# Kernel tuning notes

Measured on AMD Instinct MI355X. Metric: run time of the kernel, lower is better.

Reference implementation:

```python
import jax, jax.numpy as jnp
import numpy as np

N = 50000      # nodes
E = 800000     # edges (avg degree 16)
IN = 128       # in_feats
OUT = 128      # out_feats
ASSIGN = 256   # assign_dim = B graphs * 8 clusters
B = 32         # batch_size (num graphs)


def setup_inputs() -> dict:
    key = jax.random.key(0)
    k0, k1, k2, k3 = jax.random.split(key, 4)
    x = jax.random.normal(k0, (N, IN), jnp.float32)
    edge_index = jax.random.randint(k1, (2, E), 0, N, dtype=jnp.int32)
    # sorted graph ids, ~equal-sized graphs (mirrors block_diag mask construction)
    batch = ((jnp.arange(N, dtype=jnp.int32) * B) // N).astype(jnp.int32)
    # SAGEConv params: Linear(2*in_feats -> out) on concat([x, mean_neigh])
    W_embed = jax.random.normal(k2, (2 * IN, OUT), jnp.float32) / np.float32(np.sqrt(2 * IN))
    b_embed = jnp.zeros((OUT,), jnp.float32)
    W_pool = jax.random.normal(k3, (2 * IN, ASSIGN), jnp.float32) / np.float32(np.sqrt(2 * IN))
    b_pool = jnp.zeros((ASSIGN,), jnp.float32)
    return dict(x=x, edge_index=edge_index, batch=batch,
                W_embed=W_embed, b_embed=b_embed, W_pool=W_pool, b_pool=b_pool)


def _sage(x, src, dst, W, b):
    # mean aggregation over in-neighbors (messages src -> dst), then Linear on concat
    n = x.shape[0]
    deg = jax.ops.segment_sum(jnp.ones((src.shape[0],), x.dtype), dst, num_segments=n)
    neigh = jax.ops.segment_sum(x[src], dst, num_segments=n) / jnp.maximum(deg, 1.0)[:, None]
    return jnp.concatenate([x, neigh], axis=-1) @ W + b


def reference(x, edge_index, batch, W_embed, b_embed, W_pool, b_pool):
    src, dst = edge_index[0], edge_index[1]
    embed = _sage(x, src, dst, W_embed, b_embed)                      # [N, OUT]
    pooled = jax.nn.softmax(_sage(x, src, dst, W_pool, b_pool), -1)   # [N, ASSIGN]
    # block-diagonal mask: node i of graph g sees columns [g*C, (g+1)*C)
    C = ASSIGN // B
    cols = jnp.arange(ASSIGN, dtype=batch.dtype) // C
    mask = (batch[:, None] == cols[None, :]).astype(x.dtype)          # [N, ASSIGN]
    # NOTE: faithful to original: softmax of (mask * pooled), zeros contribute exp(0)
    r = jax.nn.softmax(mask * pooled, axis=-1) * mask
    r = r / (r.sum(axis=-1, keepdims=True) + 1e-13)                   # [N, ASSIGN]
    h = r.T @ embed                                                   # [ASSIGN, OUT]
    # adj_new = S^T A S with A sparse COO (rows=edge_index[0], cols=edge_index[1])
    ar = jax.ops.segment_sum(r[dst], src, num_segments=x.shape[0])    # A @ S : [N, ASSIGN]
    adj_new = r.T @ ar                                                # [ASSIGN, ASSIGN]
    return (adj_new, h)
```

## Files before the change

### kernel.cpp

```cpp
#include <hip/hip_runtime.h>
#include <hip/hip_bf16.h>

#define N_ 50000
#define E_ 800000
#define IN_ 128
#define OUT_ 128
#define ASSIGN_ 256
#define B_ 32
#define KTOT 256
#define JTOT 384
#define HCHUNK 32
#define ACHUNK 32
#define AST 72
#define NXP ((N_ + 127) / 128)
#define NGB (NXP * 3)
#define NCVX 6250

#define NBKT 256
#define NPB 196
#define BCAP 4000
#define EPB 4096
#define NBLK_A ((E_ + EPB - 1) / EPB)
#define NPRE (NBLK_A + NCVX + 384)

typedef __attribute__((ext_vector_type(8))) short short8;
typedef __attribute__((ext_vector_type(4))) float f32x4;
typedef __attribute__((ext_vector_type(2))) float f32x2;
typedef __attribute__((ext_vector_type(4))) unsigned short ushort4v;
typedef __attribute__((ext_vector_type(2))) unsigned short ushort2v;
typedef unsigned short u16;

__device__ inline unsigned short f2bf(float v) {
    union { float f; unsigned u; } a;
    a.f = v;
    unsigned r = a.u + 0x7fff + ((a.u >> 16) & 1);
    return (unsigned short)(r >> 16);
}
__device__ inline float bf2f(unsigned short b) {
    union { unsigned u; float f; } a;
    a.u = ((unsigned)b) << 16;
    return a.f;
}

__device__ inline unsigned enc8(float v) {
    union { float f; unsigned u; } a;
    a.f = v * 0x1p-120f;
    unsigned b = a.u;
    unsigned r = b + 0x7FFFF + ((b >> 20) & 1);
    return ((r >> 20) & 0x7F) | ((b >> 24) & 0x80);
}
__device__ inline float2 dec8x2(unsigned short p) {
#if defined(__has_builtin) && __has_builtin(__builtin_amdgcn_cvt_pk_f32_fp8)
    f32x2 r = __builtin_amdgcn_cvt_pk_f32_fp8((int)(unsigned)p, false);
    return make_float2(r.x, r.y);
#else
    unsigned u0 = p & 0xffu, u1 = (p >> 8) & 0xffu;
    union { unsigned u; float f; } a, b;
    a.u = ((u0 & 0x80u) << 24) | ((u0 & 0x7fu) << 20);
    b.u = ((u1 & 0x80u) << 24) | ((u1 & 0x7fu) << 20);
    return make_float2(a.f * 0x1p+120f, b.f * 0x1p+120f);
#endif
}

__device__ __forceinline__ void gload16(const u16* g, u16* l) {
    __builtin_amdgcn_global_load_lds(
        (const __attribute__((address_space(1))) void*)g,
        (__attribute__((address_space(3))) void*)l, 16, 0, 0);
}

__global__ __launch_bounds__(256) void k_pre(const int* __restrict__ ei,
                                             int* __restrict__ bktFill,
                                             int2* __restrict__ ebkt,
                                             const float* __restrict__ x,
                                             unsigned short* __restrict__ xhi,
                                             unsigned char* __restrict__ xq,
                                             const float* __restrict__ We,
                                             const float* __restrict__ be,
                                             const float* __restrict__ Wp,
                                             const float* __restrict__ bp,
                                             unsigned short* __restrict__ WThi,
                                             float* __restrict__ bias) {
    __shared__ int lh[NBKT], lbase[NBKT], lofs[NBKT];
    int bid = blockIdx.x;
    int t = threadIdx.x;
    if (bid < NBLK_A) {
        int e0 = bid * EPB;
        lh[t] = 0; lofs[t] = 0;
        __syncthreads();
        int ss[16], dd[16];
#pragma unroll
        for (int i = 0; i < 16; i++) {
            int e = e0 + i * 256 + t;
            ss[i] = 0; dd[i] = -1;
            if (e < E_) {
                ss[i] = ei[e];
                dd[i] = ei[E_ + e];
                atomicAdd(&lh[dd[i] / NPB], 1);
            }
        }
        __syncthreads();
        lbase[t] = t * BCAP + atomicAdd(&bktFill[t], lh[t]);
        __syncthreads();
#pragma unroll
        for (int i = 0; i < 16; i++) {
            if (dd[i] >= 0) {
                int b = dd[i] / NPB;
                int o = atomicAdd(&lofs[b], 1);
                ebkt[lbase[b] + o] = make_int2(ss[i], dd[i]);
            }
        }
        return;
    }
    if (bid >= NBLK_A + NCVX) {
        int idx = (bid - NBLK_A - NCVX) * 256 + t;
        if (idx < JTOT * KTOT) {
            int j = idx / KTOT, k = idx - j * KTOT;
            float v = (j < 128) ? We[k * 128 + j] : Wp[k * 256 + (j - 128)];
            WThi[idx] = f2bf(v);
        }
        if (idx < JTOT) bias[idx] = (idx < 128) ? be[idx] : bp[idx - 128];
        return;
    }
    int i4 = ((bid - NBLK_A) * 256 + t) * 4;
    if (i4 >= N_ * 128) return;
    float4 v = *(const float4*)(x + i4);
    ushort4v h;
    h.x = f2bf(v.x); h.y = f2bf(v.y); h.z = f2bf(v.z); h.w = f2bf(v.w);
    *(ushort4v*)(xhi + i4) = h;
    unsigned q = enc8(v.x) | (enc8(v.y) << 8) | (enc8(v.z) << 16) | (enc8(v.w) << 24);
    *(unsigned*)(xq + i4) = q;
}

__global__ __launch_bounds__(256) void k_binB(const int* __restrict__ bktFill,
                                              const int2* __restrict__ ebkt,
                                              int* __restrict__ ready,
                                              int* __restrict__ rowStart,
                                              int* __restrict__ csr_src,
                                              int* __restrict__ csr_dst) {
    __shared__ int ldeg[NPB];
    __shared__ int lscan[256];
    __shared__ int bsc[NBKT];
    __shared__ int lfill[NPB];
    int b = blockIdx.x, t = threadIdx.x;
    if (t < NPB) ldeg[t] = 0;
    __syncthreads();
    int base = b * BCAP;
    int cnt = bktFill[b];
    int n0 = b * NPB;
    for (int j = t; j < cnt; j += 256)
        atomicAdd(&ldeg[ebkt[base + j].y - n0], 1);
    __syncthreads();
    lscan[t] = (t < NPB) ? ldeg[t] : 0;
    __syncthreads();
    for (int off = 1; off < 256; off <<= 1) {
        int x0 = lscan[t];
        int a0 = (t >= off) ? lscan[t - off] : 0;
        __syncthreads();
        lscan[t] = x0 + a0;
        __syncthreads();
    }
    if (t == 0) atomicExch(&ready[b], lscan[NPB - 1] + 1);
    {
        int v;
        while ((v = atomicAdd(&ready[t], 0)) == 0) __builtin_amdgcn_s_sleep(8);
        bsc[t] = v - 1;
    }
    __syncthreads();
    for (int off = 1; off < NBKT; off <<= 1) {
        int x = bsc[t];
        int add = (t >= off) ? bsc[t - off] : 0;
        __syncthreads();
        bsc[t] = x + add;
        __syncthreads();
    }
    int base0 = (b == 0) ? 0 : bsc[b - 1];
    if (t < NPB) {
        int n = n0 + t;
        if (n < N_) {
            int excl = (t == 0) ? 0 : lscan[t - 1];
            lfill[t] = excl;
            rowStart[n] = base0 + excl;
        }
    }
    __syncthreads();
    for (int j = t; j < cnt; j += 256) {
        int2 sd = ebkt[base + j];
        int p = base0 + atomicAdd(&lfill[sd.y - n0], 1);
        csr_src[p] = sd.x;
        csr_dst[p] = sd.y;
    }
    if (b == 0 && t == 0) rowStart[N_] = E_;
}

__global__ __launch_bounds__(256) void k_agg(const unsigned char* __restrict__ xq,
                                             const int* __restrict__ rowStart,
                                             const int* __restrict__ csr_src,
                                             unsigned short* __restrict__ nhi) {
    int node = blockIdx.x * 4 + (threadIdx.x >> 6);
    if (node >= N_) return;
    int lane = threadIdx.x & 63;
    int es = lane >> 3;
    int fb = lane & 7;
    int a = rowStart[node], bnd = rowStart[node + 1];
    float acc[16];
#pragma unroll
    for (int k = 0; k < 16; k++) acc[k] = 0.f;
#define DEC(Q)                                                       \
    {                                                                \
        unsigned wq[4] = {(Q).x, (Q).y, (Q).z, (Q).w};               \
        _Pragma("unroll")                                            \
        for (int wi = 0; wi < 4; wi++) {                             \
            float2 f01 = dec8x2((unsigned short)(wq[wi] & 0xffffu)); \
            float2 f23 = dec8x2((unsigned short)(wq[wi] >> 16));     \
            acc[wi * 4 + 0] += f01.x; acc[wi * 4 + 1] += f01.y;      \
            acc[wi * 4 + 2] += f23.x; acc[wi * 4 + 3] += f23.y;      \
        }                                                            \
    }
    int j = a;
    for (; j + 8 < bnd; j += 16) {
        int s0 = csr_src[j + es];
        uint4 q0 = *(const uint4*)(xq + (size_t)s0 * 128 + fb * 16);
        uint4 q1 = {0, 0, 0, 0};
        int e1 = j + 8 + es;
        if (e1 < bnd) {
            int s1 = csr_src[e1];
            q1 = *(const uint4*)(xq + (size_t)s1 * 128 + fb * 16);
        }
        DEC(q0);
        DEC(q1);
    }
    if (j < bnd) {
        uint4 q0 = {0, 0, 0, 0};
        int e0 = j + es;
        if (e0 < bnd) {
            int s0 = csr_src[e0];
            q0 = *(const uint4*)(xq + (size_t)s0 * 128 + fb * 16);
        }
        DEC(q0);
    }
#undef DEC
#pragma unroll
    for (int k = 0; k < 16; k++) {
        acc[k] += __shfl_xor(acc[k], 8, 64);
        acc[k] += __shfl_xor(acc[k], 16, 64);
        acc[k] += __shfl_xor(acc[k], 32, 64);
    }
    float inv = 1.0f / (float)max(bnd - a, 1);
    if (es == 0) {
        short8 o0, o1;
#pragma unroll
        for (int k = 0; k < 8; k++) {
            o0[k] = (short)f2bf(acc[k] * inv);
            o1[k] = (short)f2bf(acc[k + 8] * inv);
        }
        *(short8*)(nhi + (size_t)node * 128 + fb * 16) = o0;
        *(short8*)(nhi + (size_t)node * 128 + fb * 16 + 8) = o1;
    }
}

__global__ __launch_bounds__(256) void k_gemm(const unsigned short* __restrict__ xhi,
                                              const unsigned short* __restrict__ nhi,
                                              const unsigned short* __restrict__ WThi,
                                              const float* __restrict__ bias,
                                              unsigned short* __restrict__ embed,
                                              unsigned short* __restrict__ plog) {
    __shared__ __align__(16) union {
        struct { u16 A[2][128 * 32]; u16 B[2][128 * 32]; } s;
        u16 ep[64 * 128];
    } sm;
    int t = threadIdx.x;
    int wave = t >> 6, lane = t & 63;
    int wm = wave >> 1, wn = wave & 1;
    int q = lane >> 4, lr = lane & 15;

    int id = blockIdx.x;
    int xi, cc;
    if (id < (NXP / 8) * 24) {
        xi = (id / 24) * 8 + (id & 7);
        cc = (id % 24) >> 3;
    } else {
        int r2 = id - (NXP / 8) * 24;
        xi = (NXP / 8) * 8 + r2 % (NXP % 8);
        cc = r2 / (NXP % 8);
    }
    int row0 = xi * 128;
    int col0 = cc * 128;

    f32x4 acc[4][4] = {};

    int segRow[2], segSl[2];
#pragma unroll
    for (int i = 0; i < 2; i++) {
        int R0 = (wave * 2 + i) * 16;
        segRow[i] = R0 + (lane >> 2);
        segSl[i] = (lane & 3) ^ ((segRow[i] >> 1) & 3);
    }

#define ISSUE(KT, BUF)                                                               \
    {                                                                                \
        const u16* Asrc = ((KT) < 128) ? xhi : nhi;                                  \
        int kb = (KT) & 127;                                                         \
        _Pragma("unroll")                                                            \
        for (int i = 0; i < 2; i++) {                                                \
            int nd = row0 + segRow[i];                                               \
            if (nd >= N_) nd = N_ - 1;                                               \
            gload16(Asrc + (size_t)nd * 128 + kb + segSl[i] * 8,                     \
                    &sm.s.A[BUF][((wave * 2 + i) * 16) * 32] + lane * 8);            \
            gload16(WThi + (size_t)(col0 + segRow[i]) * 256 + (KT) + segSl[i] * 8,   \
                    &sm.s.B[BUF][((wave * 2 + i) * 16) * 32] + lane * 8);            \
        }                                                                            \
    }

    ISSUE(0, 0);
    int p = 0;
    for (int kt = 0; kt < KTOT; kt += 32, p ^= 1) {
        __syncthreads();
        if (kt + 32 < KTOT) ISSUE(kt + 32, p ^ 1);

        short8 afh[4];
#pragma unroll
        for (int mi = 0; mi < 4; mi++) {
            int r = wm * 64 + mi * 16 + lr;
            afh[mi] = *(const short8*)&sm.s.A[p][r * 32 + ((q * 8) ^ (((r >> 1) & 3) * 8))];
        }
#pragma unroll
        for (int ni = 0; ni < 4; ni++) {
            int r = wn * 64 + ni * 16 + lr;
            short8 bfh = *(const short8*)&sm.s.B[p][r * 32 + ((q * 8) ^ (((r >> 1) & 3) * 8))];
#pragma unroll
            for (int mi = 0; mi < 4; mi++)
                acc[mi][ni] = __builtin_amdgcn_mfma_f32_16x16x32_bf16(afh[mi], bfh, acc[mi][ni], 0, 0, 0);
        }
    }
#undef ISSUE

    for (int half = 0; half < 2; half++) {
        __syncthreads();
        if (wm == half) {
#pragma unroll
            for (int mi = 0; mi < 4; mi++)
#pragma unroll
                for (int ni = 0; ni < 4; ni++) {
                    int lcol = wn * 64 + ni * 16 + lr;
                    float bj = bias[col0 + lcol];
#pragma unroll
                    for (int r = 0; r < 4; r++) {
                        int lrow = mi * 16 + q * 4 + r;
                        sm.ep[lrow * 128 + lcol] = f2bf(acc[mi][ni][r] + bj);
                    }
                }
        }
        __syncthreads();
#pragma unroll
        for (int i = 0; i < 4; i++) {
            int chunk = i * 256 + t;
            int lrow = chunk >> 4;
            int lco = (chunk & 15) * 8;
            int grow = row0 + half * 64 + lrow;
            if (grow < N_) {
                short8 v = *(const short8*)&sm.ep[lrow * 128 + lco];
                if (col0 < 128)
                    *(short8*)(embed + (size_t)grow * 128 + lco) = v;
                else
                    *(short8*)(plog + (size_t)grow * 256 + (col0 - 128) + lco) = v;
            }
        }
    }
}

__global__ __launch_bounds__(256) void k_r(const unsigned short* __restrict__ plog,
                                           const int* __restrict__ batch,
                                           float* __restrict__ r8,
                                           unsigned short* __restrict__ r8b) {
    int node = blockIdx.x * 4 + (threadIdx.x >> 6);
    int lane = threadIdx.x & 63;
    if (node >= N_) return;
    ushort4v p4 = *(const ushort4v*)(plog + (size_t)node * 256 + lane * 4);
    float px = bf2f(p4.x), py = bf2f(p4.y), pz = bf2f(p4.z), pw = bf2f(p4.w);
    float m = fmaxf(fmaxf(px, py), fmaxf(pz, pw));
    for (int off = 32; off; off >>= 1) m = fmaxf(m, __shfl_xor(m, off, 64));
    float s = expf(px - m) + expf(py - m) + expf(pz - m) + expf(pw - m);
    for (int off = 32; off; off >>= 1) s += __shfl_xor(s, off, 64);
    int g = batch[node];
    float v = 0.f;
    if (lane < 8) v = expf(bf2f(plog[(size_t)node * 256 + g * 8 + lane]) - m) / s;
    float M2 = v;
    for (int off = 4; off; off >>= 1) M2 = fmaxf(M2, __shfl_xor(M2, off, 64));
    float e = expf(v - M2);
    float Sg = e;
    for (int off = 4; off; off >>= 1) Sg += __shfl_xor(Sg, off, 64);
    float D2 = Sg + 248.0f * expf(-M2);
    float r = e / (Sg + 1e-13f * D2);
    if (lane < 8) {
        r8[node * 8 + lane] = r;
        r8b[node * 8 + lane] = f2bf(r);
    }
}

__global__ __launch_bounds__(256) void k_tail(const int* __restrict__ rowStart,
                                              const int* __restrict__ csr_src,
                                              const int* __restrict__ csr_dst,
                                              const unsigned short* __restrict__ r8b,
                                              float* __restrict__ partAdj,
                                              const unsigned short* __restrict__ embed,
                                              const float* __restrict__ r8,
                                              float* __restrict__ partH) {
    __shared__ __align__(16) unsigned short Ab[256 * AST];
    __shared__ __align__(16) unsigned short Bb[16 * AST];
    int id = blockIdx.x;
    int t = threadIdx.x;
    if (id >= B_ * ACHUNK) {
        int idh = id - B_ * ACHUNK;
        int g = idh & 31;
        int c = idh >> 5;
        int wv = t >> 6, l = t & 63;
        int n0g = (g * N_ + 31) >> 5;
        int n1g = ((g + 1) * N_ + 31) >> 5;
        int len = n1g - n0g;
        int a = n0g + (len * c) / HCHUNK;
        int b = n0g + (len * (c + 1)) / HCHUNK;
        float acc[8][2] = {};
        for (int n = a + wv; n < b; n += 4) {
            unsigned e2 = *(const unsigned*)(embed + (size_t)n * 128 + l * 2);
            float e0 = bf2f((u16)(e2 & 0xffffu));
            float e1 = bf2f((u16)(e2 >> 16));
            f32x4 r0 = *(const f32x4*)(r8 + n * 8);
            f32x4 r1 = *(const f32x4*)(r8 + n * 8 + 4);
#pragma unroll
            for (int c2 = 0; c2 < 4; c2++) {
                acc[c2][0] += r0[c2] * e0; acc[c2][1] += r0[c2] * e1;
                acc[c2 + 4][0] += r1[c2] * e0; acc[c2 + 4][1] += r1[c2] * e1;
            }
        }
        float* hredf = (float*)Ab;
#pragma unroll
        for (int c2 = 0; c2 < 8; c2++) {
            hredf[wv * 1024 + c2 * 128 + l * 2] = acc[c2][0];
            hredf[wv * 1024 + c2 * 128 + l * 2 + 1] = acc[c2][1];
        }
        __syncthreads();
        float* pb = partH + (g * HCHUNK + c) * 1024;
        for (int o = t; o < 1024; o += 256)
            pb[o] = (hredf[o] + hredf[1024 + o]) + (hredf[2048 + o] + hredf[3072 + o]);
        return;
    }
    int gd = id & 31;
    int c = id >> 5;
    int wave = t >> 6, lane = t & 63;
    int q = lane >> 4, lr = lane & 15;
    int n0g = (gd * N_ + 31) >> 5;
    int n1g = ((gd + 1) * N_ + 31) >> 5;
    int len = n1g - n0g;
    int na = n0g + (len * c) / ACHUNK;
    int nb = n0g + (len * (c + 1)) / ACHUNK;
    int j0 = rowStart[na], j1 = rowStart[nb];

    uint4 z = {0, 0, 0, 0};
#pragma unroll
    for (int i = 0; i < 9; i++) *(uint4*)&Ab[(i * 256 + t) * 8] = z;
    if (t < 144) *(uint4*)&Bb[t * 8] = z;
    __syncthreads();

    f32x4 acc[4] = {};
    int el = t >> 2;
    int ap = t & 3;

    int jcur = j0 + el;
    unsigned sv = 0, dv = 0;
    int gs = 0;
    bool have = jcur < j1;
    if (have) {
        int s = csr_src[jcur];
        int d = csr_dst[jcur];
        gs = (s * B_) / N_;
        sv = *(const unsigned*)(r8b + (size_t)s * 8 + ap * 2);
        dv = *(const unsigned*)(r8b + (size_t)d * 8 + ap * 2);
    }
    int pca = -1;

    for (int jt = j0; jt < j1; jt += 64) {
        if (pca >= 0) {
            Ab[pca * AST + el] = 0;
            Ab[(pca + 1) * AST + el] = 0;
            Bb[(ap * 2) * AST + el] = 0;
            Bb[(ap * 2 + 1) * AST + el] = 0;
        }
        int ca = -1;
        if (have) {
            ca = gs * 8 + ap * 2;
            Ab[ca * AST + el] = (unsigned short)sv;
            Ab[(ca + 1) * AST + el] = (unsigned short)(sv >> 16);
            Bb[(ap * 2) * AST + el] = (unsigned short)dv;
            Bb[(ap * 2 + 1) * AST + el] = (unsigned short)(dv >> 16);
        }
        __syncthreads();
        int jn = jt + 64 + el;
        bool haveN = jn < j1;
        unsigned svN = 0, dvN = 0;
        int gsN = 0;
        if (haveN) {
            int s = csr_src[jn];
            int d = csr_dst[jn];
            gsN = (s * B_) / N_;
            svN = *(const unsigned*)(r8b + (size_t)s * 8 + ap * 2);
            dvN = *(const unsigned*)(r8b + (size_t)d * 8 + ap * 2);
        }
        short8 bf0 = *(const short8*)&Bb[lr * AST + q * 8];
        short8 bf1 = *(const short8*)&Bb[lr * AST + 32 + q * 8];
#pragma unroll
        for (int mi = 0; mi < 4; mi++) {
            int col = (wave * 4 + mi) * 16 + lr;
            short8 a0 = *(const short8*)&Ab[col * AST + q * 8];
            short8 a1 = *(const short8*)&Ab[col * AST + 32 + q * 8];
            acc[mi] = __builtin_amdgcn_mfma_f32_16x16x32_bf16(a0, bf0, acc[mi], 0, 0, 0);
            acc[mi] = __builtin_amdgcn_mfma_f32_16x16x32_bf16(a1, bf1, acc[mi], 0, 0, 0);
        }
        __syncthreads();
        pca = ca;
        have = haveN; gs = gsN; sv = svN; dv = dvN;
    }

    float* pb = partAdj + (gd * ACHUNK + c) * 2048;
    if (lr < 8) {
#pragma unroll
        for (int mi = 0; mi < 4; mi++) {
            int mbase = (wave * 4 + mi) * 16 + q * 4;
#pragma unroll
            for (int r = 0; r < 4; r++)
                pb[(mbase + r) * 8 + lr] = acc[mi][r];
        }
    }
}

__global__ __launch_bounds__(256) void k_red(const float* __restrict__ partAdj,
                                             const float* __restrict__ partH,
                                             float* __restrict__ out) {
    int o = blockIdx.x * 256 + threadIdx.x;
    if (o < 256 * 256) {
        int row = o >> 8, col = o & 255;
        int gd = col >> 3, b = col & 7;
        int li = row * 8 + b;
        float s = 0.f;
#pragma unroll
        for (int c = 0; c < ACHUNK; c++) s += partAdj[(gd * ACHUNK + c) * 2048 + li];
        out[o] = s;
    } else {
        int idx = o - 256 * 256;
        int g = idx >> 10;
        int local = idx & 1023;
        float s = 0.f;
#pragma unroll
        for (int c = 0; c < HCHUNK; c++) s += partH[(g * HCHUNK + c) * 1024 + local];
        out[256 * 256 + idx] = s;
    }
}

extern "C" void kernel_launch(void* const* d_in, const int* in_sizes, int n_in,
                              void* d_out, int out_size, void* d_ws, size_t ws_size,
                              hipStream_t stream) {
    const float* x = (const float*)d_in[0];
    const int* ei = (const int*)d_in[1];
    const int* batch = (const int*)d_in[2];
    const float* We = (const float*)d_in[3];
    const float* be = (const float*)d_in[4];
    const float* Wp = (const float*)d_in[5];
    const float* bp = (const float*)d_in[6];
    float* out = (float*)d_out;

    char* w = (char*)d_ws;
    auto alloc = [&](size_t bytes) -> char* {
        char* p = w;
        w += (bytes + 255) & ~(size_t)255;
        return p;
    };
    unsigned short* xhi = (unsigned short*)alloc((size_t)N_ * 128 * 2);
    unsigned char* xq = (unsigned char*)alloc((size_t)N_ * 128);
    unsigned short* nhi = (unsigned short*)alloc((size_t)N_ * 128 * 2);
    unsigned short* WThi = (unsigned short*)alloc((size_t)JTOT * KTOT * 2);
    unsigned short* embed = (unsigned short*)alloc((size_t)N_ * 128 * 2);
    unsigned short* plog = (unsigned short*)alloc((size_t)N_ * 256 * 2);
    float* r8 = (float*)alloc((size_t)N_ * 8 * 4);
    unsigned short* r8b = (unsigned short*)alloc((size_t)N_ * 8 * 2);
    float* bias = (float*)alloc(JTOT * 4);
    int* rowStart = (int*)alloc((size_t)(N_ + 1) * 4);
    int* csr_src = (int*)alloc((size_t)E_ * 4);
    int* csr_dst = (int*)alloc((size_t)E_ * 4);
    int* flags = (int*)alloc(2 * NBKT * 4);
    int* bktFill = flags;
    int* ready = flags + NBKT;
    int2* ebkt = (int2*)alloc((size_t)NBKT * BCAP * 8);
    float* partH = (float*)alloc((size_t)B_ * HCHUNK * 1024 * 4);
    float* partAdj = (float*)alloc((size_t)B_ * ACHUNK * 2048 * 4);

    hipMemsetAsync(flags, 0, 2 * NBKT * 4, stream);
    k_pre<<<NPRE, 256, 0, stream>>>(ei, bktFill, ebkt, x, xhi, xq, We, be, Wp, bp, WThi, bias);
    k_binB<<<NBKT, 256, 0, stream>>>(bktFill, ebkt, ready, rowStart, csr_src, csr_dst);
    k_agg<<<(N_ + 3) / 4, 256, 0, stream>>>(xq, rowStart, csr_src, nhi);
    k_gemm<<<NGB, 256, 0, stream>>>(xhi, nhi, WThi, bias, embed, plog);
    k_r<<<(N_ + 3) / 4, 256, 0, stream>>>(plog, batch, r8, r8b);
    k_tail<<<2 * B_ * ACHUNK, 256, 0, stream>>>(rowStart, csr_src, csr_dst, r8b, partAdj,
                                                embed, r8, partH);
    k_red<<<(256 * 256 + 256 * 128 + 255) / 256, 256, 0, stream>>>(partAdj, partH, out);
}
```

Measured before the change: 213.2 us.

## Fuse neighbor aggregation and GEMM into one persistent kernel with panel-ready flags

Merges the aggregation and SAGE GEMM kernels into a single persistent launch. Blocks first take 4-node aggregation units from an atomic work counter and bump a per-128-row panel counter when each unit is done. They then run the GEMM, whose tiles spin-wait on that counter only before loading the neighbor half of the K dimension. The aim is to overlap the GEMM's x-half with the tail of aggregation and to drop the launch boundary. It adds spin-waiting, relies on forward progress with 4096 resident blocks, and writes nhi through relaxed atomic stores.

```diff
diff --git a/kernel.cpp b/kernel.cpp
--- a/kernel.cpp
+++ b/kernel.cpp
@@ -15,6 +15,8 @@
 #define NXP ((N_ + 127) / 128)
 #define NGB (NXP * 3)
 #define NCVX 6250
+#define NAGU 12500
+#define NAG 4096
 
 #define NBKT 256
 #define NPB 196
@@ -29,6 +31,7 @@
 typedef __attribute__((ext_vector_type(4))) unsigned short ushort4v;
 typedef __attribute__((ext_vector_type(2))) unsigned short ushort2v;
 typedef unsigned short u16;
+typedef unsigned long long u64;
 
 __device__ inline unsigned short f2bf(float v) {
     union { float f; unsigned u; } a;
@@ -192,88 +195,101 @@
     if (b == 0 && t == 0) rowStart[N_] = E_;
 }
 
-__global__ __launch_bounds__(256) void k_agg(const unsigned char* __restrict__ xq,
-                                             const int* __restrict__ rowStart,
-                                             const int* __restrict__ csr_src,
-                                             unsigned short* __restrict__ nhi) {
-    int node = blockIdx.x * 4 + (threadIdx.x >> 6);
-    if (node >= N_) return;
-    int lane = threadIdx.x & 63;
-    int es = lane >> 3;
-    int fb = lane & 7;
-    int a = rowStart[node], bnd = rowStart[node + 1];
-    float acc[16];
-#pragma unroll
-    for (int k = 0; k < 16; k++) acc[k] = 0.f;
-#define DEC(Q)                                                       \
-    {                                                                \
-        unsigned wq[4] = {(Q).x, (Q).y, (Q).z, (Q).w};               \
-        _Pragma("unroll")                                            \
-        for (int wi = 0; wi < 4; wi++) {                             \
-            float2 f01 = dec8x2((unsigned short)(wq[wi] & 0xffffu)); \
-            float2 f23 = dec8x2((unsigned short)(wq[wi] >> 16));     \
-            acc[wi * 4 + 0] += f01.x; acc[wi * 4 + 1] += f01.y;      \
-            acc[wi * 4 + 2] += f23.x; acc[wi * 4 + 3] += f23.y;      \
-        }                                                            \
-    }
-    int j = a;
-    for (; j + 8 < bnd; j += 16) {
-        int s0 = csr_src[j + es];
-        uint4 q0 = *(const uint4*)(xq + (size_t)s0 * 128 + fb * 16);
-        uint4 q1 = {0, 0, 0, 0};
-        int e1 = j + 8 + es;
-        if (e1 < bnd) {
-            int s1 = csr_src[e1];
-            q1 = *(const uint4*)(xq + (size_t)s1 * 128 + fb * 16);
-        }
-        DEC(q0);
-        DEC(q1);
-    }
-    if (j < bnd) {
-        uint4 q0 = {0, 0, 0, 0};
-        int e0 = j + es;
-        if (e0 < bnd) {
-            int s0 = csr_src[e0];
-            q0 = *(const uint4*)(xq + (size_t)s0 * 128 + fb * 16);
-        }
-        DEC(q0);
-    }
-#undef DEC
-#pragma unroll
-    for (int k = 0; k < 16; k++) {
-        acc[k] += __shfl_xor(acc[k], 8, 64);
-        acc[k] += __shfl_xor(acc[k], 16, 64);
-        acc[k] += __shfl_xor(acc[k], 32, 64);
-    }
-    float inv = 1.0f / (float)max(bnd - a, 1);
-    if (es == 0) {
-        short8 o0, o1;
-#pragma unroll
-        for (int k = 0; k < 8; k++) {
-            o0[k] = (short)f2bf(acc[k] * inv);
-            o1[k] = (short)f2bf(acc[k + 8] * inv);
-        }
-        *(short8*)(nhi + (size_t)node * 128 + fb * 16) = o0;
-        *(short8*)(nhi + (size_t)node * 128 + fb * 16 + 8) = o1;
-    }
-}
-
-__global__ __launch_bounds__(256) void k_gemm(const unsigned short* __restrict__ xhi,
-                                              const unsigned short* __restrict__ nhi,
-                                              const unsigned short* __restrict__ WThi,
-                                              const float* __restrict__ bias,
-                                              unsigned short* __restrict__ embed,
-                                              unsigned short* __restrict__ plog) {
+#define LDA 40
+__global__ __launch_bounds__(256) void k_ag(const unsigned char* __restrict__ xq,
+                                            const int* __restrict__ rowStart,
+                                            const int* __restrict__ csr_src,
+                                            unsigned short* nhi,
+                                            const unsigned short* __restrict__ xhi,
+                                            const unsigned short* __restrict__ WThi,
+                                            const float* __restrict__ bias,
+                                            unsigned short* __restrict__ embed,
+                                            unsigned short* __restrict__ plog,
+                                            int* __restrict__ aggCtr,
+                                            int* __restrict__ panelCnt) {
     __shared__ __align__(16) union {
         struct { u16 A[2][128 * 32]; u16 B[2][128 * 32]; } s;
         u16 ep[64 * 128];
     } sm;
+    __shared__ int unitSh;
     int t = threadIdx.x;
     int wave = t >> 6, lane = t & 63;
     int wm = wave >> 1, wn = wave & 1;
     int q = lane >> 4, lr = lane & 15;
-
     int id = blockIdx.x;
+
+    {
+        int es = lane >> 3;
+        int fb = lane & 7;
+        for (;;) {
+            __syncthreads();
+            if (t == 0) unitSh = atomicAdd(aggCtr, 1);
+            __syncthreads();
+            int u = unitSh;
+            if (u >= NAGU) break;
+            int node = u * 4 + wave;
+            int a = rowStart[node], bnd = rowStart[node + 1];
+            float aacc[16];
+#pragma unroll
+            for (int k = 0; k < 16; k++) aacc[k] = 0.f;
+#define DEC(Q)                                                       \
+            {                                                        \
+                unsigned wq[4] = {(Q).x, (Q).y, (Q).z, (Q).w};       \
+                _Pragma("unroll")                                    \
+                for (int wi = 0; wi < 4; wi++) {                     \
+                    float2 f01 = dec8x2((unsigned short)(wq[wi] & 0xffffu)); \
+                    float2 f23 = dec8x2((unsigned short)(wq[wi] >> 16));     \
+                    aacc[wi * 4 + 0] += f01.x; aacc[wi * 4 + 1] += f01.y;    \
+                    aacc[wi * 4 + 2] += f23.x; aacc[wi * 4 + 3] += f23.y;    \
+                }                                                    \
+            }
+            int j = a;
+            for (; j + 8 < bnd; j += 16) {
+                int s0 = csr_src[j + es];
+                uint4 q0 = *(const uint4*)(xq + (size_t)s0 * 128 + fb * 16);
+                uint4 q1 = {0, 0, 0, 0};
+                int e1 = j + 8 + es;
+                if (e1 < bnd) {
+                    int s1 = csr_src[e1];
+                    q1 = *(const uint4*)(xq + (size_t)s1 * 128 + fb * 16);
+                }
+                DEC(q0);
+                DEC(q1);
+            }
+            if (j < bnd) {
+                uint4 q0 = {0, 0, 0, 0};
+                int e0 = j + es;
+                if (e0 < bnd) {
+                    int s0 = csr_src[e0];
+                    q0 = *(const uint4*)(xq + (size_t)s0 * 128 + fb * 16);
+                }
+                DEC(q0);
+            }
+#undef DEC
+#pragma unroll
+            for (int k = 0; k < 16; k++) {
+                aacc[k] += __shfl_xor(aacc[k], 8, 64);
+                aacc[k] += __shfl_xor(aacc[k], 16, 64);
+                aacc[k] += __shfl_xor(aacc[k], 32, 64);
+            }
+            float inv = 1.0f / (float)max(bnd - a, 1);
+            if (es == 0) {
+                u64* dst = (u64*)(nhi + (size_t)node * 128 + fb * 16);
+#pragma unroll
+                for (int kk = 0; kk < 4; kk++) {
+                    u64 wv = (u64)f2bf(aacc[4 * kk + 0] * inv)
+                           | ((u64)f2bf(aacc[4 * kk + 1] * inv) << 16)
+                           | ((u64)f2bf(aacc[4 * kk + 2] * inv) << 32)
+                           | ((u64)f2bf(aacc[4 * kk + 3] * inv) << 48);
+                    __hip_atomic_store(dst + kk, wv, __ATOMIC_RELAXED, __HIP_MEMORY_SCOPE_AGENT);
+                }
+            }
+            __syncthreads();
+            if (t == 0) atomicAdd(&panelCnt[u >> 5], 1);
+        }
+    }
+    if (id >= NGB) return;
+
     int xi, cc;
     if (id < (NXP / 8) * 24) {
         xi = (id / 24) * 8 + (id & 7);
@@ -285,6 +301,7 @@
     }
     int row0 = xi * 128;
     int col0 = cc * 128;
+    int target = min(32, (N_ - row0 + 3) >> 2);
 
     f32x4 acc[4][4] = {};
 
@@ -298,7 +315,7 @@
 
 #define ISSUE(KT, BUF)                                                               \
     {                                                                                \
-        const u16* Asrc = ((KT) < 128) ? xhi : nhi;                                  \
+        const u16* Asrc = ((KT) < 128) ? xhi : (const u16*)nhi;                      \
         int kb = (KT) & 127;                                                         \
         _Pragma("unroll")                                                            \
         for (int i = 0; i < 2; i++) {                                                \
@@ -315,7 +332,15 @@
     int p = 0;
     for (int kt = 0; kt < KTOT; kt += 32, p ^= 1) {
         __syncthreads();
-        if (kt + 32 < KTOT) ISSUE(kt + 32, p ^ 1);
+        if (kt + 32 < KTOT) {
+            if (kt + 32 == 128) {
+                if (t == 0) {
+                    while (atomicAdd(&panelCnt[xi], 0) < target) __builtin_amdgcn_s_sleep(16);
+                }
+                __syncthreads();
+            }
+            ISSUE(kt + 32, p ^ 1);
+        }
 
         short8 afh[4];
 #pragma unroll
@@ -585,18 +610,20 @@
     int* rowStart = (int*)alloc((size_t)(N_ + 1) * 4);
     int* csr_src = (int*)alloc((size_t)E_ * 4);
     int* csr_dst = (int*)alloc((size_t)E_ * 4);
-    int* flags = (int*)alloc(2 * NBKT * 4);
+    int* flags = (int*)alloc((2 * NBKT + 8 + NXP) * 4);
     int* bktFill = flags;
     int* ready = flags + NBKT;
+    int* aggCtr = flags + 2 * NBKT;
+    int* panelCnt = flags + 2 * NBKT + 8;
     int2* ebkt = (int2*)alloc((size_t)NBKT * BCAP * 8);
     float* partH = (float*)alloc((size_t)B_ * HCHUNK * 1024 * 4);
     float* partAdj = (float*)alloc((size_t)B_ * ACHUNK * 2048 * 4);
 
-    hipMemsetAsync(flags, 0, 2 * NBKT * 4, stream);
+    hipMemsetAsync(flags, 0, (2 * NBKT + 8 + NXP) * 4, stream);
     k_pre<<<NPRE, 256, 0, stream>>>(ei, bktFill, ebkt, x, xhi, xq, We, be, Wp, bp, WThi, bias);
     k_binB<<<NBKT, 256, 0, stream>>>(bktFill, ebkt, ready, rowStart, csr_src, csr_dst);
-    k_agg<<<(N_ + 3) / 4, 256, 0, stream>>>(xq, rowStart, csr_src, nhi);
-    k_gemm<<<NGB, 256, 0, stream>>>(xhi, nhi, WThi, bias, embed, plog);
+    k_ag<<<NAG, 256, 0, stream>>>(xq, rowStart, csr_src, nhi, xhi, WThi, bias, embed, plog,
+                                  aggCtr, panelCnt);
     k_r<<<(N_ + 3) / 4, 256, 0, stream>>>(plog, batch, r8, r8b);
     k_tail<<<2 * B_ * ACHUNK, 256, 0, stream>>>(rowStart, csr_src, csr_dst, r8b, partAdj,
                                                 embed, r8, partH);
```

New measurement: 372.0 us. 1.74x slower.
